# Kernel optimization log

Measured on AMD Instinct MI355X. Metric: run time of the kernel, lower is better.

The kernel has to match this reference:

```python
import jax, jax.numpy as jnp
import numpy as np

N_ENT = 100000
N_REL = 200
D_IN = 128
D_HID = 128
D_OUT = 128
N_BASES = 50
N_EDGES = 800000
N_TRIPLES = 4096
BN_EPS = 1e-5


def setup_inputs() -> dict:
    key = jax.random.key(0)
    ks = jax.random.split(key, 16)
    xavier = lambda k, shape: jax.random.normal(k, shape, jnp.float32) * np.sqrt(2.0 / (shape[-2] + shape[-1]))
    inp = {
        'entity_embeds': xavier(ks[0], (N_ENT, D_IN)),
        'bases': xavier(ks[1], (N_BASES, D_IN)),
        'coefficients': xavier(ks[2], (N_REL, N_BASES)),
        'self_rel_embed': xavier(ks[3], (1, D_IN)),
        'W1': xavier(ks[4], (3, D_IN, D_HID)),
        'relw1': xavier(ks[5], (D_IN, D_HID)),
        'bn1_gamma': jnp.ones((D_HID,), jnp.float32),
        'bn1_beta': jnp.zeros((D_HID,), jnp.float32),
        'W2': xavier(ks[6], (3, D_HID, D_OUT)),
        'relw2': xavier(ks[7], (D_HID, D_OUT)),
        'bn2_gamma': jnp.ones((D_OUT,), jnp.float32),
        'bn2_beta': jnp.zeros((D_OUT,), jnp.float32),
        'ent_ids': jnp.arange(N_ENT, dtype=jnp.int32),
        'edge_index': jax.random.randint(ks[8], (2, N_EDGES), 0, N_ENT, jnp.int32),
        'edge_type': jax.random.randint(ks[9], (N_EDGES,), 0, 2 * N_REL + 1, jnp.int32),
        'y': jax.random.randint(ks[10], (N_EDGES,), 0, 3, jnp.int32),
    }
    heads = jax.random.randint(ks[11], (N_TRIPLES,), 0, N_ENT, jnp.int32)
    rels = jax.random.randint(ks[12], (N_TRIPLES,), 0, 2 * N_REL + 1, jnp.int32)
    tails = jax.random.randint(ks[13], (N_TRIPLES,), 0, N_ENT, jnp.int32)
    inp['triples'] = jnp.stack([heads, rels, tails], axis=1)
    return inp


def _compgcn_layer(x, r, edge_index, edge_type, y, W, relw, gamma, beta):
    src, dst = edge_index[0], edge_index[1]
    # message: gather neighbor & relation embeds, edge-direction-conditioned matmul
    msgs = x[src] - r[edge_type]                      # [E, d_in]
    out = jnp.zeros((msgs.shape[0], W.shape[-1]), msgs.dtype)
    for k in range(3):  # y in {0,1,2}: masked matmul instead of [E,d,d] gather
        mask = (y == k)[:, None]
        out = out + jnp.where(mask, msgs, 0.0) @ W[k]
    # scatter-add aggregation at destination nodes
    agg = jax.ops.segment_sum(out, dst, num_segments=x.shape[0])  # [N, d_out]
    # BatchNorm1d (training-mode batch statistics, biased var)
    mean = jnp.mean(agg, axis=0)
    var = jnp.mean(jnp.square(agg - mean), axis=0)
    bn = (agg - mean) * jax.lax.rsqrt(var + BN_EPS) * gamma + beta
    return jnp.tanh(bn), r @ relw


def reference(entity_embeds, bases, coefficients, self_rel_embed, W1, relw1,
              bn1_gamma, bn1_beta, W2, relw2, bn2_gamma, bn2_beta,
              ent_ids, edge_index, edge_type, y, triples):
    x = entity_embeds[ent_ids]
    r = coefficients @ bases                           # basis-composed relations
    r = jnp.concatenate([r, -r, self_rel_embed], axis=0)  # [2R+1, d]
    x, r = _compgcn_layer(x, r, edge_index, edge_type, y, W1, relw1, bn1_gamma, bn1_beta)
    x, r = _compgcn_layer(x, r, edge_index, edge_type, y, W2, relw2, bn2_gamma, bn2_beta)
    # decode: TransE-style L1 score
    h = x[triples[:, 0]]
    re = r[triples[:, 1]]
    t = x[triples[:, 2]]
    scores = jnp.sum(jnp.abs(h + re - t), axis=1)      # p=1 norm
    return scores
```

## Files before the change

### kernel.cpp

```cpp
#include <hip/hip_runtime.h>
#include <cstdint>

typedef __attribute__((ext_vector_type(8))) short short8;
typedef __attribute__((ext_vector_type(4))) float f32x4;

static __device__ __forceinline__ unsigned short f2bf(float f) {
  unsigned int u = __float_as_uint(f);
  unsigned int r = (u + 0x7FFFu + ((u >> 16) & 1u)) >> 16;
  return (unsigned short)r;
}
static __device__ __forceinline__ unsigned int pack2bf(float a, float b) {
  return (unsigned int)f2bf(a) | ((unsigned int)f2bf(b) << 16);
}
static __device__ __forceinline__ float2 bf2f(unsigned int u) {
  return make_float2(__uint_as_float(u << 16), __uint_as_float(u & 0xFFFF0000u));
}
static __device__ __forceinline__ void acc8(float* a, uint4 h, uint4 r) {
  float2 f, g;
  f = bf2f(h.x); g = bf2f(r.x); a[0] += f.x - g.x; a[1] += f.y - g.y;
  f = bf2f(h.y); g = bf2f(r.y); a[2] += f.x - g.x; a[3] += f.y - g.y;
  f = bf2f(h.z); g = bf2f(r.z); a[4] += f.x - g.x; a[5] += f.y - g.y;
  f = bf2f(h.w); g = bf2f(r.w); a[6] += f.x - g.x; a[7] += f.y - g.y;
}

__global__ __launch_bounds__(256) void k_prep(
    const float* __restrict__ coeff, const float* __restrict__ bases,
    const float* __restrict__ selfr, const float* __restrict__ relw1,
    const float* __restrict__ relw2,
    unsigned int* __restrict__ rfb, unsigned int* __restrict__ r1b,
    float* __restrict__ r2,
    const float* __restrict__ W1, const float* __restrict__ W2,
    unsigned short* __restrict__ WT1, unsigned short* __restrict__ WT2,
    const float* __restrict__ ent, const int* __restrict__ ent_ids,
    unsigned int* __restrict__ entbf,
    int* __restrict__ counts, float* __restrict__ stats,
    int nPairs, int nKeys, int cvtB, int cntB) {
  int b = blockIdx.x, tid = threadIdx.x;
  if (b < 201) {
    __shared__ float row[2][128], r1row[2][128];
    int half = tid >> 7, c = tid & 127;
    int r = 2 * b + half;
    bool ok = (r <= 400);
    if (ok) {
      float v;
      if (r == 400) {
        v = selfr[c];
      } else {
        int rr = (r < 200) ? r : r - 200;
        float s = 0.f;
#pragma unroll 10
        for (int k = 0; k < 50; ++k) s += coeff[rr * 50 + k] * bases[k * 128 + c];
        v = (r < 200) ? s : -s;
      }
      row[half][c] = v;
    }
    __syncthreads();
    if (ok && c < 64) rfb[r * 64 + c] = pack2bf(row[half][2 * c], row[half][2 * c + 1]);
    if (ok) {
      float s = 0.f;
#pragma unroll 8
      for (int k = 0; k < 128; ++k) s += row[half][k] * relw1[k * 128 + c];
      r1row[half][c] = s;
    }
    __syncthreads();
    if (ok && c < 64) r1b[r * 64 + c] = pack2bf(r1row[half][2 * c], r1row[half][2 * c + 1]);
    if (ok) {
      float s = 0.f;
#pragma unroll 8
      for (int k = 0; k < 128; ++k) s += r1row[half][k] * relw2[k * 128 + c];
      r2[r * 128 + c] = s;
    }
  } else if (b < 585) {
    int idx = (b - 201) * 256 + tid;
    const int half = 128 * 384;
    const float* W = (idx < half) ? W1 : W2;
    unsigned short* WT = (idx < half) ? WT1 : WT2;
    int id2 = (idx < half) ? idx : idx - half;
    int n = id2 & 127, k = id2 >> 7;
    int kk = k >> 7, kr = k & 127;
    WT[(size_t)n * 384 + k] = f2bf(W[(size_t)kk * 16384 + kr * 128 + n]);
  } else if (b < 585 + cvtB) {
    int i = (b - 585) * 256 + tid;
    if (i < nPairs) {
      int e = i >> 6;
      int src = ent_ids[e];
      float2 v = *(const float2*)&ent[(size_t)src * 128 + (i & 63) * 2];
      entbf[i] = pack2bf(v.x, v.y);
    }
  } else if (b < 585 + cvtB + cntB) {
    int i = (b - (585 + cvtB)) * 256 + tid;
    if (i < nKeys) counts[i] = 0;
  } else {
    int i = (b - (585 + cvtB + cntB)) * 256 + tid;
    if (i < 16896) stats[i] = 0.f;
  }
}

__global__ __launch_bounds__(256) void k_histR(const int* __restrict__ ei, const int* __restrict__ y,
                                               int* __restrict__ counts, int nE, int rsz) {
  int r = blockIdx.x;
  int e0 = blockIdx.y * 1024;
#pragma unroll
  for (int i = 0; i < 4; ++i) {
    int e = e0 + i * 256 + threadIdx.x;
    if (e < nE) {
      int key = ei[nE + e] * 3 + y[e];
      if (key / rsz == r) atomicAdd(&counts[key], 1);
    }
  }
}

__global__ __launch_bounds__(256) void k_fillR(const int* __restrict__ ei, const int* __restrict__ et,
                                               const int* __restrict__ y, int* __restrict__ cursor,
                                               unsigned int* __restrict__ bucket, int nE, int rsz) {
  int r = blockIdx.x;
  int e0 = blockIdx.y * 1024;
#pragma unroll
  for (int i = 0; i < 4; ++i) {
    int e = e0 + i * 256 + threadIdx.x;
    if (e < nE) {
      int key = ei[nE + e] * 3 + y[e];
      if (key / rsz == r) {
        int slot = atomicAdd(&cursor[key], 1);
        bucket[slot] = (unsigned int)ei[e] | ((unsigned int)et[e] << 20);
      }
    }
  }
}

__global__ void k_scan1(const int* __restrict__ counts, int* __restrict__ local,
                        int* __restrict__ blockSums, int n) {
  __shared__ int sdata[1024];
  int tid = threadIdx.x;
  int i = blockIdx.x * 1024 + tid;
  int v = (i < n) ? counts[i] : 0;
  sdata[tid] = v;
  __syncthreads();
  for (int off = 1; off < 1024; off <<= 1) {
    int t = (tid >= off) ? sdata[tid - off] : 0;
    __syncthreads();
    sdata[tid] += t;
    __syncthreads();
  }
  if (i < n) local[i] = sdata[tid] - v;
  if (tid == 1023) blockSums[blockIdx.x] = sdata[1023];
}

__global__ void k_scan2(const int* __restrict__ blockSums, int* __restrict__ carries,
                        int* __restrict__ offsets, int n, int nb) {
  __shared__ int sdata[1024];
  int tid = threadIdx.x;
  int v = (tid < nb) ? blockSums[tid] : 0;
  sdata[tid] = v;
  __syncthreads();
  for (int off = 1; off < 1024; off <<= 1) {
    int t = (tid >= off) ? sdata[tid - off] : 0;
    __syncthreads();
    sdata[tid] += t;
    __syncthreads();
  }
  if (tid < nb) carries[tid] = sdata[tid] - v;
  if (tid == 1023) offsets[n] = sdata[1023];
}

__global__ void k_scan3(const int* __restrict__ local, const int* __restrict__ carries,
                        int* __restrict__ offsets, int* __restrict__ cursor, int n) {
  int i = blockIdx.x * 1024 + threadIdx.x;
  if (i >= n) return;
  int v = local[i] + carries[blockIdx.x];
  offsets[i] = v;
  cursor[i] = v;
}

__global__ __launch_bounds__(256, 6) void k_fused(
    const unsigned int* __restrict__ xb, const unsigned int* __restrict__ rb,
    const int* __restrict__ offsets, const unsigned int* __restrict__ packed,
    const unsigned short* __restrict__ WT, unsigned short* __restrict__ C,
    float* __restrict__ statsRep, int M) {
  __shared__ unsigned short As[32][392];
  const int tid = threadIdx.x;
  const int m0 = blockIdx.x * 32;
  const int wave = tid >> 6, lane = tid & 63;
  const int quad = lane >> 4, l16 = lane & 15;
  const int qid = (wave << 2) | quad;

  {
    const int dst0 = m0 + 2 * qid;
    int b0, b1, b2, b3, b4, b5, b6;
    if (dst0 + 1 < M) {
      const int base = dst0 * 3;
      b0 = offsets[base];     b1 = offsets[base + 1];
      b2 = offsets[base + 2]; b3 = offsets[base + 3];
      b4 = offsets[base + 4]; b5 = offsets[base + 5];
      b6 = offsets[base + 6];
    } else if (dst0 < M) {
      const int base = dst0 * 3;
      b0 = offsets[base];     b1 = offsets[base + 1];
      b2 = offsets[base + 2]; b3 = offsets[base + 3];
      b4 = b3; b5 = b3; b6 = b3;
    } else {
      b0 = b1 = b2 = b3 = b4 = b5 = b6 = 0;
    }
    float ac[8] = {};
    int seg = 0;
    int nextB = b1;
    int j = b0;
    const int hi = b6;
    unsigned short* lds0 = &As[2 * qid][0];

    auto flushSeg = [&]() {
      int rowOff = (seg >= 3) ? 392 : 0;
      int cls = seg - ((seg >= 3) ? 3 : 0);
      uint4 ov;
      ov.x = pack2bf(ac[0], ac[1]);
      ov.y = pack2bf(ac[2], ac[3]);
      ov.z = pack2bf(ac[4], ac[5]);
      ov.w = pack2bf(ac[6], ac[7]);
      *(uint4*)(lds0 + rowOff + cls * 128 + l16 * 8) = ov;
#pragma unroll
      for (int z = 0; z < 8; ++z) ac[z] = 0.f;
      ++seg;
      nextB = (seg == 1) ? b2 : (seg == 2) ? b3 : (seg == 3) ? b4
            : (seg == 4) ? b5 : b6;
    };

    if (j < hi) {
      int jc1 = (j + 1 < hi) ? j + 1 : j;
      unsigned int q0 = packed[j], q1 = packed[jc1];
      int s0 = q0 & 0xFFFFF, t0 = q0 >> 20;
      int s1 = q1 & 0xFFFFF, t1 = q1 >> 20;
      uint4 h0 = *(const uint4*)&xb[(size_t)s0 * 64 + l16 * 4];
      uint4 r0 = *(const uint4*)&rb[(size_t)t0 * 64 + l16 * 4];
      uint4 h1 = *(const uint4*)&xb[(size_t)s1 * 64 + l16 * 4];
      uint4 r1 = *(const uint4*)&rb[(size_t)t1 * 64 + l16 * 4];
      while (j < hi) {
        int jp2 = (j + 2 < hi) ? j + 2 : hi - 1;
        int jp3 = (j + 3 < hi) ? j + 3 : hi - 1;
        unsigned int q2 = packed[jp2], q3 = packed[jp3];
        int s2 = q2 & 0xFFFFF, t2 = q2 >> 20;
        int s3 = q3 & 0xFFFFF, t3 = q3 >> 20;
        uint4 th0 = *(const uint4*)&xb[(size_t)s2 * 64 + l16 * 4];
        uint4 tr0 = *(const uint4*)&rb[(size_t)t2 * 64 + l16 * 4];
        uint4 th1 = *(const uint4*)&xb[(size_t)s3 * 64 + l16 * 4];
        uint4 tr1 = *(const uint4*)&rb[(size_t)t3 * 64 + l16 * 4];
        while (j == nextB) flushSeg();
        acc8(ac, h0, r0);
        ++j;
        if (j < hi) {
          while (j == nextB) flushSeg();
          acc8(ac, h1, r1);
          ++j;
        }
        h0 = th0; r0 = tr0; h1 = th1; r1 = tr1;
      }
    }
    while (seg < 6) flushSeg();
  }
  __syncthreads();

  const unsigned short* Wp = WT + (size_t)(wave * 32 + l16) * 384 + quad * 8;
  short8 bc0 = *(const short8*)(Wp);
  short8 bc1 = *(const short8*)(Wp + 16 * 384);
  f32x4 acc[2][2] = {};
#pragma unroll 1
  for (int it = 0; it < 12; ++it) {
    short8 bn0, bn1;
    if (it < 11) {
      bn0 = *(const short8*)(Wp + (it + 1) * 32);
      bn1 = *(const short8*)(Wp + 16 * 384 + (it + 1) * 32);
    }
    short8 a0 = *(const short8*)&As[l16][it * 32 + quad * 8];
    short8 a1 = *(const short8*)&As[16 + l16][it * 32 + quad * 8];
    acc[0][0] = __builtin_amdgcn_mfma_f32_16x16x32_bf16(a0, bc0, acc[0][0], 0, 0, 0);
    acc[0][1] = __builtin_amdgcn_mfma_f32_16x16x32_bf16(a0, bc1, acc[0][1], 0, 0, 0);
    acc[1][0] = __builtin_amdgcn_mfma_f32_16x16x32_bf16(a1, bc0, acc[1][0], 0, 0, 0);
    acc[1][1] = __builtin_amdgcn_mfma_f32_16x16x32_bf16(a1, bc1, acc[1][1], 0, 0, 0);
    if (it < 11) { bc0 = bn0; bc1 = bn1; }
  }

  float ps[2] = {}, pq[2] = {};
#pragma unroll
  for (int t = 0; t < 2; ++t)
#pragma unroll
    for (int reg = 0; reg < 4; ++reg) {
      int m = m0 + t * 16 + quad * 4 + reg;
      if (m < M) {
#pragma unroll
        for (int ct = 0; ct < 2; ++ct) {
          float v = acc[t][ct][reg];
          int col = wave * 32 + ct * 16 + l16;
          C[(size_t)m * 128 + col] = f2bf(v);
          ps[ct] += v; pq[ct] += v * v;
        }
      }
    }
#pragma unroll
  for (int ct = 0; ct < 2; ++ct) {
    ps[ct] += __shfl_xor(ps[ct], 16);
    ps[ct] += __shfl_xor(ps[ct], 32);
    pq[ct] += __shfl_xor(pq[ct], 16);
    pq[ct] += __shfl_xor(pq[ct], 32);
  }
  if (quad == 0) {
    float* rep = statsRep + ((blockIdx.x & 31) << 8);
#pragma unroll
    for (int ct = 0; ct < 2; ++ct) {
      int col = wave * 32 + ct * 16 + l16;
      atomicAdd(&rep[col], ps[ct]);
      atomicAdd(&rep[128 + col], pq[ct]);
    }
  }
}

__global__ void k_norm(const uint4* __restrict__ Cb4, const float* __restrict__ rep,
                       const float* __restrict__ gamma, const float* __restrict__ beta,
                       float invN, uint4* __restrict__ xb4, int nQuad) {
  __shared__ float sc_s[128], bi_s[128];
  if (threadIdx.x < 128) {
    int c = threadIdx.x;
    float s = 0.f, q = 0.f;
#pragma unroll
    for (int r = 0; r < 32; ++r) {
      s += rep[r * 256 + c];
      q += rep[r * 256 + 128 + c];
    }
    float mean = s * invN;
    float var = fmaxf(q * invN - mean * mean, 0.f);
    float sc = rsqrtf(var + 1e-5f) * gamma[c];
    sc_s[c] = sc;
    bi_s[c] = beta[c] - mean * sc;
  }
  __syncthreads();
  int i = blockIdx.x * blockDim.x + threadIdx.x;
  if (i >= nQuad) return;
  uint4 v = Cb4[i];
  int j = (i * 4) & 63;
  uint4 o;
  float2 f;
  f = bf2f(v.x);
  o.x = pack2bf(tanhf(fmaf(f.x, sc_s[2*j],   bi_s[2*j])),   tanhf(fmaf(f.y, sc_s[2*j+1], bi_s[2*j+1])));
  f = bf2f(v.y);
  o.y = pack2bf(tanhf(fmaf(f.x, sc_s[2*j+2], bi_s[2*j+2])), tanhf(fmaf(f.y, sc_s[2*j+3], bi_s[2*j+3])));
  f = bf2f(v.z);
  o.z = pack2bf(tanhf(fmaf(f.x, sc_s[2*j+4], bi_s[2*j+4])), tanhf(fmaf(f.y, sc_s[2*j+5], bi_s[2*j+5])));
  f = bf2f(v.w);
  o.w = pack2bf(tanhf(fmaf(f.x, sc_s[2*j+6], bi_s[2*j+6])), tanhf(fmaf(f.y, sc_s[2*j+7], bi_s[2*j+7])));
  xb4[i] = o;
}

__global__ void k_score(const unsigned int* __restrict__ xb, const float* __restrict__ r,
                        const int* __restrict__ triples, float* __restrict__ out, int nT) {
  int gid = blockIdx.x * blockDim.x + threadIdx.x;
  int t = gid >> 6;
  if (t >= nT) return;
  int lane = gid & 63;
  int h = triples[t * 3], rel = triples[t * 3 + 1], tl = triples[t * 3 + 2];
  float2 a = bf2f(xb[(size_t)h * 64 + lane]);
  float2 b = *(const float2*)&r[(size_t)rel * 128 + lane * 2];
  float2 cc = bf2f(xb[(size_t)tl * 64 + lane]);
  float s = fabsf(a.x + b.x - cc.x) + fabsf(a.y + b.y - cc.y);
#pragma unroll
  for (int off = 32; off > 0; off >>= 1) s += __shfl_down(s, off);
  if (lane == 0) out[t] = s;
}

extern "C" void kernel_launch(void* const* d_in, const int* in_sizes, int n_in,
                              void* d_out, int out_size, void* d_ws, size_t ws_size,
                              hipStream_t stream) {
  const float* ent   = (const float*)d_in[0];
  const float* bases = (const float*)d_in[1];
  const float* coeff = (const float*)d_in[2];
  const float* selfr = (const float*)d_in[3];
  const float* W1    = (const float*)d_in[4];
  const float* relw1 = (const float*)d_in[5];
  const float* g1    = (const float*)d_in[6];
  const float* b1    = (const float*)d_in[7];
  const float* W2    = (const float*)d_in[8];
  const float* relw2 = (const float*)d_in[9];
  const float* g2    = (const float*)d_in[10];
  const float* b2    = (const float*)d_in[11];
  const int* ent_ids = (const int*)d_in[12];
  const int* ei      = (const int*)d_in[13];
  const int* et      = (const int*)d_in[14];
  const int* yk      = (const int*)d_in[15];
  const int* triples = (const int*)d_in[16];

  const int M  = in_sizes[0] / 128;
  const int nE = in_sizes[14];
  const int nT = in_sizes[16] / 3;
  const int nKeys = M * 3;
  const int nScanBlocks = (nKeys + 1023) / 1024;
  const int rsz = (nKeys + 7) / 8;

  float* p = (float*)d_ws;
  float* r2    = p; p += 401 * 128;
  float* statsAll = p; p += 16896;
  float* rep1 = statsAll;
  float* rep2 = statsAll + 32 * 256;
  unsigned short* Cb  = (unsigned short*)p;
  unsigned int* entbf = (unsigned int*)(Cb + (size_t)M * 128);
  unsigned int* xb    = entbf + (size_t)M * 64;
  unsigned int* rfb   = xb + (size_t)M * 64;
  unsigned int* r1b   = rfb + 401 * 64;
  unsigned short* WT1 = (unsigned short*)(r1b + 401 * 64);
  unsigned short* WT2 = WT1 + 128 * 384;
  int* counts  = (int*)(WT2 + 128 * 384);
  int* offsets = counts + nKeys;
  int* cursor  = offsets + nKeys + 1;
  int* slocal  = cursor + nKeys;
  int* sblock  = slocal + nKeys;
  int* scarry  = sblock + nScanBlocks;
  unsigned int* bucket = (unsigned int*)(scarry + nScanBlocks);

  float* out = (float*)d_out;

  const int nPairs = M * 64;
  const int nQuad  = M * 16;
  const int cvtB = (nPairs + 255) / 256;
  const int cntB = (nKeys + 255) / 256;
  const int zeroB = 66;
  const int prepBlocks = 585 + cvtB + cntB + zeroB;
  const int fusedBlocks = (M + 31) / 32;
  const int normBlocks = (nQuad + 255) / 256;
  const dim3 rangedGrid(8, (nE + 1023) / 1024);

  k_prep<<<prepBlocks, 256, 0, stream>>>(coeff, bases, selfr, relw1, relw2,
                                         rfb, r1b, r2, W1, W2, WT1, WT2,
                                         ent, ent_ids, entbf, counts, statsAll,
                                         nPairs, nKeys, cvtB, cntB);

  k_histR<<<rangedGrid, 256, 0, stream>>>(ei, yk, counts, nE, rsz);
  k_scan1<<<nScanBlocks, 1024, 0, stream>>>(counts, slocal, sblock, nKeys);
  k_scan2<<<1, 1024, 0, stream>>>(sblock, scarry, offsets, nKeys, nScanBlocks);
  k_scan3<<<nScanBlocks, 1024, 0, stream>>>(slocal, scarry, offsets, cursor, nKeys);
  k_fillR<<<rangedGrid, 256, 0, stream>>>(ei, et, yk, cursor, bucket, nE, rsz);

  k_fused<<<fusedBlocks, 256, 0, stream>>>(entbf, rfb, offsets, bucket, WT1,
                                           Cb, rep1, M);
  k_norm<<<normBlocks, 256, 0, stream>>>((const uint4*)Cb, rep1, g1, b1,
                                         1.0f / M, (uint4*)xb, nQuad);

  k_fused<<<fusedBlocks, 256, 0, stream>>>(xb, r1b, offsets, bucket, WT2,
                                           Cb, rep2, M);
  k_norm<<<normBlocks, 256, 0, stream>>>((const uint4*)Cb, rep2, g2, b2,
                                         1.0f / M, (uint4*)xb, nQuad);

  k_score<<<(nT * 64 + 255) / 256, 256, 0, stream>>>(xb, r2, triples, out, nT);
}
```

Measured before the change: 387.7 us.

## Precompute edge keys/payloads once and fold final BN+tanh into scoring

```diff
diff --git a/kernel.cpp b/kernel.cpp
--- a/kernel.cpp
+++ b/kernel.cpp
@@ -34,7 +34,10 @@
     const float* __restrict__ ent, const int* __restrict__ ent_ids,
     unsigned int* __restrict__ entbf,
     int* __restrict__ counts, float* __restrict__ stats,
-    int nPairs, int nKeys, int cvtB, int cntB) {
+    const int* __restrict__ ei, const int* __restrict__ et,
+    const int* __restrict__ yk, int* __restrict__ keyA,
+    unsigned int* __restrict__ payA, int nE,
+    int nPairs, int nKeys, int cvtB, int cntB, int zeroB) {
   int b = blockIdx.x, tid = threadIdx.x;
   if (b < 201) {
     __shared__ float row[2][128], r1row[2][128];
@@ -90,13 +93,22 @@
   } else if (b < 585 + cvtB + cntB) {
     int i = (b - (585 + cvtB)) * 256 + tid;
     if (i < nKeys) counts[i] = 0;
-  } else {
+  } else if (b < 585 + cvtB + cntB + zeroB) {
     int i = (b - (585 + cvtB + cntB)) * 256 + tid;
     if (i < 16896) stats[i] = 0.f;
-  }
-}
-
-__global__ __launch_bounds__(256) void k_histR(const int* __restrict__ ei, const int* __restrict__ y,
+  } else {
+    int e = (b - (585 + cvtB + cntB + zeroB)) * 1024 + tid;
+#pragma unroll
+    for (int i = 0; i < 4; ++i, e += 256) {
+      if (e < nE) {
+        keyA[e] = ei[nE + e] * 3 + yk[e];
+        payA[e] = (unsigned int)ei[e] | ((unsigned int)et[e] << 20);
+      }
+    }
+  }
+}
+
+__global__ __launch_bounds__(256) void k_histR(const int* __restrict__ keyA,
                                                int* __restrict__ counts, int nE, int rsz) {
   int r = blockIdx.x;
   int e0 = blockIdx.y * 1024;
@@ -104,14 +116,15 @@
   for (int i = 0; i < 4; ++i) {
     int e = e0 + i * 256 + threadIdx.x;
     if (e < nE) {
-      int key = ei[nE + e] * 3 + y[e];
+      int key = keyA[e];
       if (key / rsz == r) atomicAdd(&counts[key], 1);
     }
   }
 }
 
-__global__ __launch_bounds__(256) void k_fillR(const int* __restrict__ ei, const int* __restrict__ et,
-                                               const int* __restrict__ y, int* __restrict__ cursor,
+__global__ __launch_bounds__(256) void k_fillR(const int* __restrict__ keyA,
+                                               const unsigned int* __restrict__ payA,
+                                               int* __restrict__ cursor,
                                                unsigned int* __restrict__ bucket, int nE, int rsz) {
   int r = blockIdx.x;
   int e0 = blockIdx.y * 1024;
@@ -119,10 +132,10 @@
   for (int i = 0; i < 4; ++i) {
     int e = e0 + i * 256 + threadIdx.x;
     if (e < nE) {
-      int key = ei[nE + e] * 3 + y[e];
+      int key = keyA[e];
       if (key / rsz == r) {
         int slot = atomicAdd(&cursor[key], 1);
-        bucket[slot] = (unsigned int)ei[e] | ((unsigned int)et[e] << 20);
+        bucket[slot] = payA[e];
       }
     }
   }
@@ -348,17 +361,39 @@
   xb4[i] = o;
 }
 
-__global__ void k_score(const unsigned int* __restrict__ xb, const float* __restrict__ r,
+__global__ void k_score(const unsigned int* __restrict__ Cbu, const float* __restrict__ rep,
+                        const float* __restrict__ gamma, const float* __restrict__ beta,
+                        float invN, const float* __restrict__ r,
                         const int* __restrict__ triples, float* __restrict__ out, int nT) {
+  __shared__ float sc_s[128], bi_s[128];
+  if (threadIdx.x < 128) {
+    int c = threadIdx.x;
+    float s = 0.f, q = 0.f;
+#pragma unroll
+    for (int rr = 0; rr < 32; ++rr) {
+      s += rep[rr * 256 + c];
+      q += rep[rr * 256 + 128 + c];
+    }
+    float mean = s * invN;
+    float var = fmaxf(q * invN - mean * mean, 0.f);
+    float sc = rsqrtf(var + 1e-5f) * gamma[c];
+    sc_s[c] = sc;
+    bi_s[c] = beta[c] - mean * sc;
+  }
+  __syncthreads();
   int gid = blockIdx.x * blockDim.x + threadIdx.x;
   int t = gid >> 6;
   if (t >= nT) return;
   int lane = gid & 63;
   int h = triples[t * 3], rel = triples[t * 3 + 1], tl = triples[t * 3 + 2];
-  float2 a = bf2f(xb[(size_t)h * 64 + lane]);
+  float2 a = bf2f(Cbu[(size_t)h * 64 + lane]);
   float2 b = *(const float2*)&r[(size_t)rel * 128 + lane * 2];
-  float2 cc = bf2f(xb[(size_t)tl * 64 + lane]);
-  float s = fabsf(a.x + b.x - cc.x) + fabsf(a.y + b.y - cc.y);
+  float2 cc = bf2f(Cbu[(size_t)tl * 64 + lane]);
+  float ax = tanhf(fmaf(a.x, sc_s[2 * lane], bi_s[2 * lane]));
+  float ay = tanhf(fmaf(a.y, sc_s[2 * lane + 1], bi_s[2 * lane + 1]));
+  float cx = tanhf(fmaf(cc.x, sc_s[2 * lane], bi_s[2 * lane]));
+  float cy = tanhf(fmaf(cc.y, sc_s[2 * lane + 1], bi_s[2 * lane + 1]));
+  float s = fabsf(ax + b.x - cx) + fabsf(ay + b.y - cy);
 #pragma unroll
   for (int off = 32; off > 0; off >>= 1) s += __shfl_down(s, off);
   if (lane == 0) out[t] = s;
@@ -411,6 +446,8 @@
   int* sblock  = slocal + nKeys;
   int* scarry  = sblock + nScanBlocks;
   unsigned int* bucket = (unsigned int*)(scarry + nScanBlocks);
+  int* keyA = (int*)(bucket + nE);
+  unsigned int* payA = (unsigned int*)(keyA + nE);
 
   float* out = (float*)d_out;
 
@@ -419,7 +456,8 @@
   const int cvtB = (nPairs + 255) / 256;
   const int cntB = (nKeys + 255) / 256;
   const int zeroB = 66;
-  const int prepBlocks = 585 + cvtB + cntB + zeroB;
+  const int kpB = (nE + 1023) / 1024;
+  const int prepBlocks = 585 + cvtB + cntB + zeroB + kpB;
   const int fusedBlocks = (M + 31) / 32;
   const int normBlocks = (nQuad + 255) / 256;
   const dim3 rangedGrid(8, (nE + 1023) / 1024);
@@ -427,13 +465,14 @@
   k_prep<<<prepBlocks, 256, 0, stream>>>(coeff, bases, selfr, relw1, relw2,
                                          rfb, r1b, r2, W1, W2, WT1, WT2,
                                          ent, ent_ids, entbf, counts, statsAll,
-                                         nPairs, nKeys, cvtB, cntB);
-
-  k_histR<<<rangedGrid, 256, 0, stream>>>(ei, yk, counts, nE, rsz);
+                                         ei, et, yk, keyA, payA, nE,
+                                         nPairs, nKeys, cvtB, cntB, zeroB);
+
+  k_histR<<<rangedGrid, 256, 0, stream>>>(keyA, counts, nE, rsz);
   k_scan1<<<nScanBlocks, 1024, 0, stream>>>(counts, slocal, sblock, nKeys);
   k_scan2<<<1, 1024, 0, stream>>>(sblock, scarry, offsets, nKeys, nScanBlocks);
   k_scan3<<<nScanBlocks, 1024, 0, stream>>>(slocal, scarry, offsets, cursor, nKeys);
-  k_fillR<<<rangedGrid, 256, 0, stream>>>(ei, et, yk, cursor, bucket, nE, rsz);
+  k_fillR<<<rangedGrid, 256, 0, stream>>>(keyA, payA, cursor, bucket, nE, rsz);
 
   k_fused<<<fusedBlocks, 256, 0, stream>>>(entbf, rfb, offsets, bucket, WT1,
                                            Cb, rep1, M);
@@ -442,8 +481,8 @@
 
   k_fused<<<fusedBlocks, 256, 0, stream>>>(xb, r1b, offsets, bucket, WT2,
                                            Cb, rep2, M);
-  k_norm<<<normBlocks, 256, 0, stream>>>((const uint4*)Cb, rep2, g2, b2,
-                                         1.0f / M, (uint4*)xb, nQuad);
-
-  k_score<<<(nT * 64 + 255) / 256, 256, 0, stream>>>(xb, r2, triples, out, nT);
-}
+
+  k_score<<<(nT * 64 + 255) / 256, 256, 0, stream>>>((const unsigned int*)Cb, rep2,
+                                                     g2, b2, 1.0f / M, r2,
+                                                     triples, out, nT);
+}
```

Result: faster. 375.5 us (-3.1%).
